# Kernel tuning notes

Measured on AMD Instinct MI355X. Metric: run time of the kernel, lower is better.

Reference implementation:

```python
import jax, jax.numpy as jnp
import numpy as np

N_NODES = 100000
N_EDGES = 600000
EMB = 128
L = 5
NUM_ATOM = 119
NUM_CHIR = 3
NUM_BTYPE = 5
NUM_BDIR = 3
BN_EPS = 1e-5


def setup_inputs() -> dict:
    key = jax.random.key(0)
    ks = jax.random.split(key, 16)
    inp = {}
    inp['x'] = jax.random.randint(ks[0], (N_NODES, 2), 0, NUM_ATOM, dtype=jnp.int64 if jax.config.jax_enable_x64 else jnp.int32)
    inp['edge_index'] = jax.random.randint(ks[1], (2, N_EDGES), 0, N_NODES)
    inp['edge_attr'] = jax.random.randint(ks[2], (N_EDGES, 2), 0, NUM_BDIR)
    s = 0.05
    inp['x_emb1'] = jax.random.normal(ks[3], (NUM_ATOM, EMB), jnp.float32) * s
    inp['x_emb2'] = jax.random.normal(ks[4], (NUM_CHIR, EMB), jnp.float32) * s
    inp['edge_emb1'] = jax.random.normal(ks[5], (L, NUM_BTYPE, EMB), jnp.float32) * s
    inp['edge_emb2'] = jax.random.normal(ks[6], (L, NUM_BDIR, EMB), jnp.float32) * s
    inp['W1'] = jax.random.normal(ks[7], (L, EMB, 2 * EMB), jnp.float32) * (1.0 / np.sqrt(EMB))
    inp['b1'] = jnp.zeros((L, 2 * EMB), jnp.float32)
    inp['W2'] = jax.random.normal(ks[8], (L, 2 * EMB, EMB), jnp.float32) * (1.0 / np.sqrt(2 * EMB))
    inp['b2'] = jnp.zeros((L, EMB), jnp.float32)
    inp['eps'] = jnp.zeros((L,), jnp.float32)
    inp['gamma'] = jnp.ones((L, EMB), jnp.float32)
    inp['beta'] = jnp.zeros((L, EMB), jnp.float32)
    return inp


def reference(x, edge_index, edge_attr, x_emb1, x_emb2, edge_emb1, edge_emb2,
              W1, b1, W2, b2, eps, gamma, beta):
    N = x.shape[0]
    # node embedding: sum of two table lookups
    x0 = jnp.clip(x[:, 0], 0, x_emb1.shape[0] - 1)
    x1 = jnp.clip(x[:, 1], 0, x_emb2.shape[0] - 1)
    h = x_emb1[x0] + x_emb2[x1]  # [N, EMB]
    # add self loops (loop edge_attr = zeros -> bond type 0 / dir 0)
    loop = jnp.arange(N, dtype=edge_index.dtype)
    src = jnp.concatenate([edge_index[0], loop])  # [E+N]
    dst = jnp.concatenate([edge_index[1], loop])
    ea = jnp.concatenate([edge_attr, jnp.zeros((N, 2), dtype=edge_attr.dtype)], axis=0)
    e0 = jnp.clip(ea[:, 0], 0, edge_emb1.shape[1] - 1)
    e1 = jnp.clip(ea[:, 1], 0, edge_emb2.shape[1] - 1)
    n_layers = eps.shape[0]
    for i in range(n_layers):
        e = edge_emb1[i][e0] + edge_emb2[i][e1]              # [E+N, EMB]
        m = jax.nn.relu(h[src] + e)                           # gather + elementwise
        agg = jax.ops.segment_sum(m, dst, num_segments=N)     # scatter-add
        out = (1.0 + eps[i]) * h + agg
        # MLP: Linear -> ReLU -> Linear
        hmid = jax.nn.relu(out @ W1[i] + b1[i])
        h = hmid @ W2[i] + b2[i]
        # BatchNorm1d over nodes (batch statistics, biased variance)
        mean = jnp.mean(h, axis=0)
        var = jnp.mean((h - mean) ** 2, axis=0)
        h = (h - mean) * jax.lax.rsqrt(var + BN_EPS) * gamma[i] + beta[i]
        if i < n_layers - 1:
            h = jax.nn.relu(h)
    return h
```

## Files before the change

### kernel.cpp

```cpp
#include <hip/hip_runtime.h>

#define NN 100000
#define NPAD 100096
#define NE 600000
#define EMB 128

typedef unsigned short u16;
typedef unsigned int u32;
typedef unsigned long long u64;
typedef _Float16 half8 __attribute__((ext_vector_type(8)));
typedef float f32x4 __attribute__((ext_vector_type(4)));

__device__ __forceinline__ float4 ld4(const float* p) { return *(const float4*)p; }
__device__ __forceinline__ u32 packh2(float a, float b) {
  union { _Float16 h[2]; u32 d; } u;
  u.h[0] = (_Float16)a;
  u.h[1] = (_Float16)b;
  return u.d;
}

__global__ __launch_bounds__(256) void node_init_kernel(
    const int* __restrict__ x, const float* __restrict__ emb1,
    const float* __restrict__ emb2, _Float16* __restrict__ hb) {
  int tid = blockIdx.x * blockDim.x + threadIdx.x;
  int n = tid >> 4;
  if (n >= NN) return;
  int kc = tid & 15;
  int x0 = min(max(x[2 * n], 0), 118);
  int x1 = min(max(x[2 * n + 1], 0), 2);
  const float* p1 = emb1 + (size_t)x0 * EMB + kc * 8;
  const float* p2 = emb2 + (size_t)x1 * EMB + kc * 8;
  _Float16 o[8];
#pragma unroll
  for (int j = 0; j < 8; ++j) o[j] = (_Float16)(p1[j] + p2[j]);
  *(ulonglong2*)(hb + (size_t)n * EMB + kc * 8) = *(ulonglong2*)o;
}

__global__ __launch_bounds__(256) void hist_kernel(const int* __restrict__ ei,
                                                   int* __restrict__ deg) {
  int e = blockIdx.x * blockDim.x + threadIdx.x;
  if (e >= NE) return;
  atomicAdd(&deg[ei[NE + e]], 1);
}

__global__ __launch_bounds__(256) void scan1_kernel(const int* __restrict__ deg,
                                                    int* __restrict__ off,
                                                    int* __restrict__ bsum,
                                                    int* __restrict__ gbins) {
  __shared__ int s[256];
  __shared__ int l[33];
  int t = threadIdx.x;
  if (t < 33) l[t] = 0;
  int base = blockIdx.x * 1024 + t * 4;
  int v[4];
#pragma unroll
  for (int j = 0; j < 4; ++j) {
    int idx = base + j;
    v[j] = (idx < NN) ? deg[idx] : 0;
  }
  int tsum = v[0] + v[1] + v[2] + v[3];
  s[t] = tsum;
  __syncthreads();
  for (int d = 1; d < 256; d <<= 1) {
    int add = (t >= d) ? s[t - d] : 0;
    __syncthreads();
    s[t] += add;
    __syncthreads();
  }
  int run = s[t] - tsum;
#pragma unroll
  for (int j = 0; j < 4; ++j) {
    int idx = base + j;
    if (idx < NN) {
      off[idx] = run;
      atomicAdd(&l[32 - min(v[j], 32)], 1);
    }
    run += v[j];
  }
  if (t == 255) bsum[blockIdx.x] = s[255];
  __syncthreads();
  if (t < 33 && l[t]) atomicAdd(&gbins[t], l[t]);
}

__global__ void scan2_kernel(int* __restrict__ bsum, int* __restrict__ off, int nb,
                             int* __restrict__ gbins) {
  int t = threadIdx.x;
  if (t < 64) {
    int lane = t;
    int v0 = (lane < nb) ? bsum[lane] : 0;
    int v1 = (lane + 64 < nb) ? bsum[lane + 64] : 0;
    int s0 = v0, s1 = v1;
    for (int d = 1; d < 64; d <<= 1) {
      int t0 = __shfl_up(s0, d);
      int t1 = __shfl_up(s1, d);
      if (lane >= d) { s0 += t0; s1 += t1; }
    }
    int tot0 = __shfl(s0, 63);
    int tot1 = __shfl(s1, 63);
    if (lane < nb) bsum[lane] = s0 - v0;
    if (lane + 64 < nb) bsum[lane + 64] = tot0 + s1 - v1;
    if (lane == 0) off[NN] = tot0 + tot1;
  } else {
    int lane = t - 64;
    int v = (lane < 33) ? gbins[lane] : 0;
    int s = v;
    for (int d = 1; d < 64; d <<= 1) {
      int tt = __shfl_up(s, d);
      if (lane >= d) s += tt;
    }
    if (lane < 33) gbins[lane] = s - v;
  }
}

__global__ __launch_bounds__(256) void scan3_kernel(int* __restrict__ off,
                                                    const int* __restrict__ bsum,
                                                    const int* __restrict__ deg,
                                                    int* __restrict__ gbins,
                                                    int* __restrict__ perm) {
  __shared__ int lcnt[33], lbase[33];
  int t = threadIdx.x;
  if (t < 33) lcnt[t] = 0;
  __syncthreads();
  int idx = blockIdx.x * 256 + t;
  int b = 0, r = 0;
  if (idx < NN) {
    off[idx] += bsum[idx >> 10];
    b = 32 - min(deg[idx], 32);
    r = atomicAdd(&lcnt[b], 1);
  }
  __syncthreads();
  if (t < 33) lbase[t] = lcnt[t] ? atomicAdd(&gbins[t], lcnt[t]) : 0;
  __syncthreads();
  if (idx < NN) perm[lbase[b] + r] = idx;
}

__global__ __launch_bounds__(256) void scatter_kernel(
    const int* __restrict__ ei, const int* __restrict__ ea,
    const int* __restrict__ off, int* __restrict__ cnt, int* __restrict__ csr) {
  int e = blockIdx.x * blockDim.x + threadIdx.x;
  if (e >= NE) return;
  int d = ei[NE + e];
  int s = ei[e];
  int a0 = min(max(ea[2 * e], 0), 4);
  int a1 = min(max(ea[2 * e + 1], 0), 2);
  int code = a0 * 3 + a1;
  int r = atomicAdd(&cnt[d], 1);
  csr[off[d] + r] = s | (code << 20);
}

__global__ __launch_bounds__(256) void prep_kernel(
    const float* __restrict__ W1g, const float* __restrict__ W2g,
    const float* __restrict__ ee1, const float* __restrict__ ee2,
    _Float16* __restrict__ W1f, _Float16* __restrict__ W2f,
    _Float16* __restrict__ cbh) {
  int idx = blockIdx.x * blockDim.x + threadIdx.x;
  _Float16 o[8];
  if (idx < 20480) {
    int lane = idx & 63;
    int r = idx >> 6;
    int nt = r & 3, kt = (r >> 2) & 3, c = (r >> 4) & 3, l = r >> 6;
    int n = c * 64 + nt * 16 + (lane & 15);
    int kb = kt * 32 + (lane >> 4) * 8;
#pragma unroll
    for (int j = 0; j < 8; ++j) o[j] = (_Float16)W1g[((size_t)l * 128 + kb + j) * 256 + n];
    *(ulonglong2*)(W1f + (size_t)idx * 8) = *(ulonglong2*)o;
  } else if (idx < 40960) {
    int i2 = idx - 20480;
    int lane = i2 & 63;
    int r = i2 >> 6;
    int nt = r & 7, ktl = (r >> 3) & 1, c = (r >> 4) & 3, l = r >> 6;
    int n = nt * 16 + (lane & 15);
    int kb = c * 64 + ktl * 32 + (lane >> 4) * 8;
#pragma unroll
    for (int j = 0; j < 8; ++j) o[j] = (_Float16)W2g[((size_t)l * 256 + kb + j) * 128 + n];
    *(ulonglong2*)(W2f + (size_t)i2 * 8) = *(ulonglong2*)o;
  } else if (idx < 40960 + 9600) {
    int i3 = idx - 40960;
    int l = i3 / (15 * 128);
    int rem = i3 % (15 * 128);
    int code = rem / 128;
    int f = rem % 128;
    cbh[i3] = (_Float16)(ee1[(l * 5 + code / 3) * 128 + f] + ee2[(l * 3 + code % 3) * 128 + f]);
  }
}

template <bool NORM>
__global__ __launch_bounds__(256) void agg_kernel(
    const _Float16* __restrict__ hsrc, const float* __restrict__ slots,
    const float* __restrict__ gamma, const float* __restrict__ beta,
    const int* __restrict__ off, const int* __restrict__ csr,
    const _Float16* __restrict__ cbh, const float* __restrict__ epsp,
    const int* __restrict__ perm, _Float16* __restrict__ Af) {
  __shared__ float s_sc[128], s_sh[128];
  int t = threadIdx.x;
  if (NORM) {
    if (t < 128) {
      float s = 0.f, s2 = 0.f;
#pragma unroll 8
      for (int k = 0; k < 32; ++k) {
        s += slots[k * 256 + t];
        s2 += slots[k * 256 + 128 + t];
      }
      float mean = s * (1.0f / NN);
      float var = s2 * (1.0f / NN) - mean * mean;
      float sc = gamma[t] * rsqrtf(var + 1e-5f);
      s_sc[t] = sc;
      s_sh[t] = beta[t] - mean * sc;
    }
    __syncthreads();
  }
  int tid = blockIdx.x * blockDim.x + t;
  int g = tid >> 4;
  int kc = tid & 15;
  float av[8] = {0.f, 0.f, 0.f, 0.f, 0.f, 0.f, 0.f, 0.f};
  float scv[8], shv[8];
  if (NORM) {
#pragma unroll
    for (int j = 0; j < 8; ++j) {
      scv[j] = s_sc[kc * 8 + j];
      shv[j] = s_sh[kc * 8 + j];
    }
  }
  int node = g;
  if (g < NN) {
    node = perm[g];
    const float eps1 = 1.0f + *epsp;
    ulonglong2 hraw = *(const ulonglong2*)(hsrc + (size_t)node * EMB + kc * 8);
    _Float16* hr = (_Float16*)&hraw;
    half8 c0 = *(const half8*)(cbh + kc * 8);
#pragma unroll
    for (int j = 0; j < 8; ++j) {
      float hv = (float)hr[j];
      if (NORM) hv = fmaxf(hv * scv[j] + shv[j], 0.f);
      av[j] = eps1 * hv + fmaxf(hv + (float)c0[j], 0.f);
    }
    int s0 = off[node], s1 = off[node + 1];
    int e = s0;
    for (; e + 3 < s1; e += 4) {
      int p0 = csr[e], p1 = csr[e + 1], p2 = csr[e + 2], p3 = csr[e + 3];
      ulonglong2 r0 = *(const ulonglong2*)(hsrc + (size_t)(p0 & 0xFFFFF) * EMB + kc * 8);
      ulonglong2 r1 = *(const ulonglong2*)(hsrc + (size_t)(p1 & 0xFFFFF) * EMB + kc * 8);
      ulonglong2 r2 = *(const ulonglong2*)(hsrc + (size_t)(p2 & 0xFFFFF) * EMB + kc * 8);
      ulonglong2 r3 = *(const ulonglong2*)(hsrc + (size_t)(p3 & 0xFFFFF) * EMB + kc * 8);
      ulonglong2 rr[4] = {r0, r1, r2, r3};
      int pp[4] = {p0, p1, p2, p3};
#pragma unroll
      for (int u = 0; u < 4; ++u) {
        half8 cc = *(const half8*)(cbh + (size_t)(pp[u] >> 20) * EMB + kc * 8);
        _Float16* sp = (_Float16*)&rr[u];
#pragma unroll
        for (int j = 0; j < 8; ++j) {
          float v = (float)sp[j];
          if (NORM) v = fmaxf(v * scv[j] + shv[j], 0.f);
          av[j] += fmaxf(v + (float)cc[j], 0.f);
        }
      }
    }
    for (; e < s1; ++e) {
      int p0 = csr[e];
      ulonglong2 r0 = *(const ulonglong2*)(hsrc + (size_t)(p0 & 0xFFFFF) * EMB + kc * 8);
      half8 cc = *(const half8*)(cbh + (size_t)(p0 >> 20) * EMB + kc * 8);
      _Float16* sp = (_Float16*)&r0;
#pragma unroll
      for (int j = 0; j < 8; ++j) {
        float v = (float)sp[j];
        if (NORM) v = fmaxf(v * scv[j] + shv[j], 0.f);
        av[j] += fmaxf(v + (float)cc[j], 0.f);
      }
    }
  }
  _Float16 o[8];
#pragma unroll
  for (int j = 0; j < 8; ++j) o[j] = (_Float16)av[j];
  *(ulonglong2*)(Af + (size_t)node * EMB + kc * 8) = *(ulonglong2*)o;
}

__global__ __launch_bounds__(256, 4) void mlp_kernel(
    const _Float16* __restrict__ Af, const _Float16* __restrict__ W1f,
    const _Float16* __restrict__ W2f,
    const float* __restrict__ b1g, const float* __restrict__ b2g,
    _Float16* __restrict__ hpre, float* __restrict__ slots) {
  __shared__ __align__(16) _Float16 Ws[16 * 64 * 8];

  const int t = threadIdx.x;
  const int w = t >> 6;
  const int lane = t & 63;
  const int q = lane >> 4, l15 = lane & 15;
  const int gw = blockIdx.x * 4 + w;
  const int n0 = gw * 16;
  float* sums = slots + (size_t)(gw & 31) * 256;

  half8 nh[4];
#pragma unroll
  for (int kt = 0; kt < 4; ++kt)
    nh[kt] = *(const half8*)(Af + (size_t)(n0 + l15) * EMB + kt * 32 + q * 8);

  f32x4 oacc[8];
#pragma unroll
  for (int a = 0; a < 8; ++a) oacc[a] = (f32x4){0.f, 0.f, 0.f, 0.f};

  const int srcA = ((q & 1) * 2) * 16 + l15;
  const int srcB = srcA + 16;
  const bool sel = (q >> 1) != 0;

  for (int c = 0; c < 4; ++c) {
    __syncthreads();
    {
      const _Float16* gb = W1f + ((size_t)(c * 16 + w * 4) * 64 + lane) * 8;
#pragma unroll
      for (int j = 0; j < 4; ++j)
        *(ulonglong2*)&Ws[(w * 4 + j) * 512 + lane * 8] =
            *(const ulonglong2*)(gb + (size_t)j * 512);
    }
    __syncthreads();

    f32x4 hacc[4];
#pragma unroll
    for (int a = 0; a < 4; ++a) hacc[a] = (f32x4){0.f, 0.f, 0.f, 0.f};
#pragma unroll
    for (int kt = 0; kt < 4; ++kt) {
#pragma unroll
      for (int colt = 0; colt < 4; ++colt) {
        half8 wh = *(const half8*)&Ws[(kt * 4 + colt) * 512 + lane * 8];
        hacc[colt] = __builtin_amdgcn_mfma_f32_16x16x32_f16(wh, nh[kt], hacc[colt], 0, 0, 0);
      }
    }
    __syncthreads();

    {
      const _Float16* gb = W2f + ((size_t)(c * 16 + w * 4) * 64 + lane) * 8;
#pragma unroll
      for (int j = 0; j < 4; ++j)
        *(ulonglong2*)&Ws[(w * 4 + j) * 512 + lane * 8] =
            *(const ulonglong2*)(gb + (size_t)j * 512);
    }

    u32 P01[4], P23[4];
#pragma unroll
    for (int colt = 0; colt < 4; ++colt) {
      float4 b1v = ld4(b1g + c * 64 + colt * 16 + q * 4);
      float v0 = fmaxf(hacc[colt][0] + b1v.x, 0.f);
      float v1 = fmaxf(hacc[colt][1] + b1v.y, 0.f);
      float v2 = fmaxf(hacc[colt][2] + b1v.z, 0.f);
      float v3 = fmaxf(hacc[colt][3] + b1v.w, 0.f);
      P01[colt] = packh2(v0, v1);
      P23[colt] = packh2(v2, v3);
    }
    __syncthreads();

#pragma unroll
    for (int ktl = 0; ktl < 2; ++ktl) {
      half8 bh;
      {
        union { u32 d[4]; half8 s; } uh;
        int c0 = 2 * ktl, c1 = 2 * ktl + 1;
        u32 a0, a1;
        a0 = (u32)__shfl((int)P01[c0], srcA); a1 = (u32)__shfl((int)P01[c1], srcA);
        uh.d[0] = sel ? a1 : a0;
        a0 = (u32)__shfl((int)P23[c0], srcA); a1 = (u32)__shfl((int)P23[c1], srcA);
        uh.d[1] = sel ? a1 : a0;
        a0 = (u32)__shfl((int)P01[c0], srcB); a1 = (u32)__shfl((int)P01[c1], srcB);
        uh.d[2] = sel ? a1 : a0;
        a0 = (u32)__shfl((int)P23[c0], srcB); a1 = (u32)__shfl((int)P23[c1], srcB);
        uh.d[3] = sel ? a1 : a0;
        bh = uh.s;
      }
#pragma unroll
      for (int nt = 0; nt < 8; ++nt) {
        half8 wh = *(const half8*)&Ws[(ktl * 8 + nt) * 512 + lane * 8];
        oacc[nt] = __builtin_amdgcn_mfma_f32_16x16x32_f16(wh, bh, oacc[nt], 0, 0, 0);
      }
    }
  }

  const int node = n0 + l15;
#pragma unroll
  for (int nt = 0; nt < 8; ++nt) {
    int ocb = nt * 16 + q * 4;
    float4 b2v = ld4(b2g + ocb);
    f32x4 s = (f32x4){0.f, 0.f, 0.f, 0.f};
    f32x4 s2 = (f32x4){0.f, 0.f, 0.f, 0.f};
    if (node < NN) {
      float v0 = oacc[nt][0] + b2v.x;
      float v1 = oacc[nt][1] + b2v.y;
      float v2 = oacc[nt][2] + b2v.z;
      float v3 = oacc[nt][3] + b2v.w;
      u64 pk = (u64)packh2(v0, v1) | ((u64)packh2(v2, v3) << 32);
      *(u64*)(hpre + (size_t)node * EMB + ocb) = pk;
      s[0] = v0; s[1] = v1; s[2] = v2; s[3] = v3;
      s2[0] = v0 * v0; s2[1] = v1 * v1; s2[2] = v2 * v2; s2[3] = v3 * v3;
    }
#pragma unroll
    for (int d = 1; d < 16; d <<= 1) {
#pragma unroll
      for (int r = 0; r < 4; ++r) {
        s[r] += __shfl_xor(s[r], d);
        s2[r] += __shfl_xor(s2[r], d);
      }
    }
    if (l15 == 0) {
#pragma unroll
      for (int r = 0; r < 4; ++r) {
        atomicAdd(&sums[ocb + r], s[r]);
        atomicAdd(&sums[128 + ocb + r], s2[r]);
      }
    }
  }
}

__global__ __launch_bounds__(256) void out_kernel(
    const _Float16* __restrict__ hpre, const float* __restrict__ slots,
    const float* __restrict__ gamma, const float* __restrict__ beta,
    float* __restrict__ out) {
  __shared__ float s_sc[128], s_sh[128];
  int t = threadIdx.x;
  if (t < 128) {
    float s = 0.f, s2 = 0.f;
#pragma unroll 8
    for (int k = 0; k < 32; ++k) {
      s += slots[k * 256 + t];
      s2 += slots[k * 256 + 128 + t];
    }
    float mean = s * (1.0f / NN);
    float var = s2 * (1.0f / NN) - mean * mean;
    float sc = gamma[t] * rsqrtf(var + 1e-5f);
    s_sc[t] = sc;
    s_sh[t] = beta[t] - mean * sc;
  }
  __syncthreads();
  int tid = blockIdx.x * blockDim.x + t;
  int n = tid >> 4;
  if (n >= NN) return;
  int kc = tid & 15;
  ulonglong2 raw = *(const ulonglong2*)(hpre + (size_t)n * EMB + kc * 8);
  _Float16* hr = (_Float16*)&raw;
  float v[8];
#pragma unroll
  for (int j = 0; j < 8; ++j) v[j] = (float)hr[j] * s_sc[kc * 8 + j] + s_sh[kc * 8 + j];
  float* d = out + (size_t)n * EMB + kc * 8;
  *(float4*)d = make_float4(v[0], v[1], v[2], v[3]);
  *(float4*)(d + 4) = make_float4(v[4], v[5], v[6], v[7]);
}

extern "C" void kernel_launch(void* const* d_in, const int* in_sizes, int n_in,
                              void* d_out, int out_size, void* d_ws, size_t ws_size,
                              hipStream_t stream) {
  const int* x = (const int*)d_in[0];
  const int* ei = (const int*)d_in[1];
  const int* ea = (const int*)d_in[2];
  const float* x_emb1 = (const float*)d_in[3];
  const float* x_emb2 = (const float*)d_in[4];
  const float* ee1 = (const float*)d_in[5];
  const float* ee2 = (const float*)d_in[6];
  const float* W1 = (const float*)d_in[7];
  const float* b1 = (const float*)d_in[8];
  const float* W2 = (const float*)d_in[9];
  const float* b2 = (const float*)d_in[10];
  const float* eps = (const float*)d_in[11];
  const float* gamma = (const float*)d_in[12];
  const float* beta = (const float*)d_in[13];
  float* out = (float*)d_out;

  float* slots = (float*)d_ws;
  _Float16* hpre = (_Float16*)(slots + 5 * 32 * 256);
  _Float16* Af = hpre + (size_t)NN * EMB;
  _Float16* hb = Af + (size_t)NPAD * EMB;
  _Float16* W1f = hb + (size_t)NN * EMB;
  _Float16* W2f = W1f + 5 * 32768;
  _Float16* cbh = W2f + 5 * 32768;
  int* deg = (int*)(cbh + 5 * 15 * 128 + 64);
  int* off = deg + NN;
  int* csr = off + NN + 1;
  int* bsum = csr + NE;
  int* gbins = bsum + 128;
  int* perm = gbins + 64;

  const int NB_SCAN = (NN + 1023) / 1024;

  hipMemsetAsync(deg, 0, NN * sizeof(int), stream);
  hipMemsetAsync(gbins, 0, 64 * sizeof(int), stream);
  hipMemsetAsync(slots, 0, 5 * 32 * 256 * sizeof(float), stream);
  hist_kernel<<<(NE + 255) / 256, 256, 0, stream>>>(ei, deg);
  scan1_kernel<<<NB_SCAN, 256, 0, stream>>>(deg, off, bsum, gbins);
  scan2_kernel<<<1, 128, 0, stream>>>(bsum, off, NB_SCAN, gbins);
  scan3_kernel<<<(NN + 255) / 256, 256, 0, stream>>>(off, bsum, deg, gbins, perm);
  hipMemsetAsync(deg, 0, NN * sizeof(int), stream);
  scatter_kernel<<<(NE + 255) / 256, 256, 0, stream>>>(ei, ea, off, deg, csr);
  prep_kernel<<<(40960 + 9600 + 255) / 256, 256, 0, stream>>>(W1, W2, ee1, ee2, W1f,
                                                              W2f, cbh);
  node_init_kernel<<<NN * 16 / 256 + 1, 256, 0, stream>>>(x, x_emb1, x_emb2, hb);

  const int NBLK = NPAD / 64;
  for (int i = 0; i < 5; ++i) {
    if (i == 0)
      agg_kernel<false><<<NPAD * 16 / 256, 256, 0, stream>>>(
          hb, nullptr, nullptr, nullptr, off, csr, cbh + (size_t)i * 15 * EMB,
          eps + i, perm, Af);
    else
      agg_kernel<true><<<NPAD * 16 / 256, 256, 0, stream>>>(
          hpre, slots + (size_t)(i - 1) * 32 * 256, gamma + (size_t)(i - 1) * EMB,
          beta + (size_t)(i - 1) * EMB, off, csr, cbh + (size_t)i * 15 * EMB,
          eps + i, perm, Af);
    mlp_kernel<<<NBLK, 256, 0, stream>>>(
        Af, W1f + (size_t)i * 32768, W2f + (size_t)i * 32768,
        b1 + (size_t)i * 256, b2 + (size_t)i * 128, hpre,
        slots + (size_t)i * 32 * 256);
  }
  out_kernel<<<NN * 16 / 256 + 1, 256, 0, stream>>>(
      hpre, slots + 4 * 32 * 256, gamma + 4 * EMB, beta + 4 * EMB, out);
}
```

Baseline: 651.2 us.

## Fuse neighbor aggregation into MLP kernel via shared-memory staging

Merges the gather/aggregate kernel into the MLP kernel. Each wave aggregates its 16 nodes straight into LDS, and the MFMA operands are loaded from LDS instead of a global Af buffer. Ping-pong hidden-state buffers avoid read/write hazards now that aggregation and output share one kernel. This removes the Af round-trip to global memory and one launch per layer. The cost is less parallelism and latency hiding for the irregular gather inside a register-heavy MFMA kernel.

```diff
diff --git a/kernel.cpp b/kernel.cpp
--- a/kernel.cpp
+++ b/kernel.cpp
@@ -185,102 +185,17 @@
 }
 
 template <bool NORM>
-__global__ __launch_bounds__(256) void agg_kernel(
-    const _Float16* __restrict__ hsrc, const float* __restrict__ slots,
+__global__ __launch_bounds__(256, 4) void fused_kernel(
+    const _Float16* __restrict__ hsrc, const float* __restrict__ slots_prev,
     const float* __restrict__ gamma, const float* __restrict__ beta,
     const int* __restrict__ off, const int* __restrict__ csr,
     const _Float16* __restrict__ cbh, const float* __restrict__ epsp,
-    const int* __restrict__ perm, _Float16* __restrict__ Af) {
+    const int* __restrict__ perm,
+    const _Float16* __restrict__ W1f, const _Float16* __restrict__ W2f,
+    const float* __restrict__ b1g, const float* __restrict__ b2g,
+    _Float16* __restrict__ hout, float* __restrict__ slots_out) {
+  __shared__ __align__(16) _Float16 Ws[16 * 64 * 8];
   __shared__ float s_sc[128], s_sh[128];
-  int t = threadIdx.x;
-  if (NORM) {
-    if (t < 128) {
-      float s = 0.f, s2 = 0.f;
-#pragma unroll 8
-      for (int k = 0; k < 32; ++k) {
-        s += slots[k * 256 + t];
-        s2 += slots[k * 256 + 128 + t];
-      }
-      float mean = s * (1.0f / NN);
-      float var = s2 * (1.0f / NN) - mean * mean;
-      float sc = gamma[t] * rsqrtf(var + 1e-5f);
-      s_sc[t] = sc;
-      s_sh[t] = beta[t] - mean * sc;
-    }
-    __syncthreads();
-  }
-  int tid = blockIdx.x * blockDim.x + t;
-  int g = tid >> 4;
-  int kc = tid & 15;
-  float av[8] = {0.f, 0.f, 0.f, 0.f, 0.f, 0.f, 0.f, 0.f};
-  float scv[8], shv[8];
-  if (NORM) {
-#pragma unroll
-    for (int j = 0; j < 8; ++j) {
-      scv[j] = s_sc[kc * 8 + j];
-      shv[j] = s_sh[kc * 8 + j];
-    }
-  }
-  int node = g;
-  if (g < NN) {
-    node = perm[g];
-    const float eps1 = 1.0f + *epsp;
-    ulonglong2 hraw = *(const ulonglong2*)(hsrc + (size_t)node * EMB + kc * 8);
-    _Float16* hr = (_Float16*)&hraw;
-    half8 c0 = *(const half8*)(cbh + kc * 8);
-#pragma unroll
-    for (int j = 0; j < 8; ++j) {
-      float hv = (float)hr[j];
-      if (NORM) hv = fmaxf(hv * scv[j] + shv[j], 0.f);
-      av[j] = eps1 * hv + fmaxf(hv + (float)c0[j], 0.f);
-    }
-    int s0 = off[node], s1 = off[node + 1];
-    int e = s0;
-    for (; e + 3 < s1; e += 4) {
-      int p0 = csr[e], p1 = csr[e + 1], p2 = csr[e + 2], p3 = csr[e + 3];
-      ulonglong2 r0 = *(const ulonglong2*)(hsrc + (size_t)(p0 & 0xFFFFF) * EMB + kc * 8);
-      ulonglong2 r1 = *(const ulonglong2*)(hsrc + (size_t)(p1 & 0xFFFFF) * EMB + kc * 8);
-      ulonglong2 r2 = *(const ulonglong2*)(hsrc + (size_t)(p2 & 0xFFFFF) * EMB + kc * 8);
-      ulonglong2 r3 = *(const ulonglong2*)(hsrc + (size_t)(p3 & 0xFFFFF) * EMB + kc * 8);
-      ulonglong2 rr[4] = {r0, r1, r2, r3};
-      int pp[4] = {p0, p1, p2, p3};
-#pragma unroll
-      for (int u = 0; u < 4; ++u) {
-        half8 cc = *(const half8*)(cbh + (size_t)(pp[u] >> 20) * EMB + kc * 8);
-        _Float16* sp = (_Float16*)&rr[u];
-#pragma unroll
-        for (int j = 0; j < 8; ++j) {
-          float v = (float)sp[j];
-          if (NORM) v = fmaxf(v * scv[j] + shv[j], 0.f);
-          av[j] += fmaxf(v + (float)cc[j], 0.f);
-        }
-      }
-    }
-    for (; e < s1; ++e) {
-      int p0 = csr[e];
-      ulonglong2 r0 = *(const ulonglong2*)(hsrc + (size_t)(p0 & 0xFFFFF) * EMB + kc * 8);
-      half8 cc = *(const half8*)(cbh + (size_t)(p0 >> 20) * EMB + kc * 8);
-      _Float16* sp = (_Float16*)&r0;
-#pragma unroll
-      for (int j = 0; j < 8; ++j) {
-        float v = (float)sp[j];
-        if (NORM) v = fmaxf(v * scv[j] + shv[j], 0.f);
-        av[j] += fmaxf(v + (float)cc[j], 0.f);
-      }
-    }
-  }
-  _Float16 o[8];
-#pragma unroll
-  for (int j = 0; j < 8; ++j) o[j] = (_Float16)av[j];
-  *(ulonglong2*)(Af + (size_t)node * EMB + kc * 8) = *(ulonglong2*)o;
-}
-
-__global__ __launch_bounds__(256, 4) void mlp_kernel(
-    const _Float16* __restrict__ Af, const _Float16* __restrict__ W1f,
-    const _Float16* __restrict__ W2f,
-    const float* __restrict__ b1g, const float* __restrict__ b2g,
-    _Float16* __restrict__ hpre, float* __restrict__ slots) {
-  __shared__ __align__(16) _Float16 Ws[16 * 64 * 8];
 
   const int t = threadIdx.x;
   const int w = t >> 6;
@@ -288,12 +203,97 @@
   const int q = lane >> 4, l15 = lane & 15;
   const int gw = blockIdx.x * 4 + w;
   const int n0 = gw * 16;
-  float* sums = slots + (size_t)(gw & 31) * 256;
+  float* sums = slots_out + (size_t)(gw & 31) * 256;
+
+  if (NORM) {
+    if (t < 128) {
+      float s = 0.f, s2 = 0.f;
+#pragma unroll 8
+      for (int k = 0; k < 32; ++k) {
+        s += slots_prev[k * 256 + t];
+        s2 += slots_prev[k * 256 + 128 + t];
+      }
+      float mean = s * (1.0f / NN);
+      float var = s2 * (1.0f / NN) - mean * mean;
+      float sc = gamma[t] * rsqrtf(var + 1e-5f);
+      s_sc[t] = sc;
+      s_sh[t] = beta[t] - mean * sc;
+    }
+    __syncthreads();
+  }
+
+  {
+    const int sub = q;
+    const int kc = l15;
+    float scv[8], shv[8];
+    if (NORM) {
+#pragma unroll
+      for (int j = 0; j < 8; ++j) {
+        scv[j] = s_sc[kc * 8 + j];
+        shv[j] = s_sh[kc * 8 + j];
+      }
+    }
+    const float eps1 = 1.0f + *epsp;
+    half8 c0 = *(const half8*)(cbh + kc * 8);
+    for (int p = 0; p < 4; ++p) {
+      int g = n0 + p * 4 + sub;
+      float av[8] = {0.f, 0.f, 0.f, 0.f, 0.f, 0.f, 0.f, 0.f};
+      if (g < NN) {
+        int node = perm[g];
+        ulonglong2 hraw = *(const ulonglong2*)(hsrc + (size_t)node * EMB + kc * 8);
+        _Float16* hr = (_Float16*)&hraw;
+#pragma unroll
+        for (int j = 0; j < 8; ++j) {
+          float hv = (float)hr[j];
+          if (NORM) hv = fmaxf(hv * scv[j] + shv[j], 0.f);
+          av[j] = eps1 * hv + fmaxf(hv + (float)c0[j], 0.f);
+        }
+        int s0 = off[node], s1 = off[node + 1];
+        int e = s0;
+        for (; e + 3 < s1; e += 4) {
+          int p0 = csr[e], p1 = csr[e + 1], p2 = csr[e + 2], p3 = csr[e + 3];
+          ulonglong2 r0 = *(const ulonglong2*)(hsrc + (size_t)(p0 & 0xFFFFF) * EMB + kc * 8);
+          ulonglong2 r1 = *(const ulonglong2*)(hsrc + (size_t)(p1 & 0xFFFFF) * EMB + kc * 8);
+          ulonglong2 r2 = *(const ulonglong2*)(hsrc + (size_t)(p2 & 0xFFFFF) * EMB + kc * 8);
+          ulonglong2 r3 = *(const ulonglong2*)(hsrc + (size_t)(p3 & 0xFFFFF) * EMB + kc * 8);
+          ulonglong2 rr[4] = {r0, r1, r2, r3};
+          int pp[4] = {p0, p1, p2, p3};
+#pragma unroll
+          for (int u = 0; u < 4; ++u) {
+            half8 cc = *(const half8*)(cbh + (size_t)(pp[u] >> 20) * EMB + kc * 8);
+            _Float16* sp = (_Float16*)&rr[u];
+#pragma unroll
+            for (int j = 0; j < 8; ++j) {
+              float v = (float)sp[j];
+              if (NORM) v = fmaxf(v * scv[j] + shv[j], 0.f);
+              av[j] += fmaxf(v + (float)cc[j], 0.f);
+            }
+          }
+        }
+        for (; e < s1; ++e) {
+          int p0 = csr[e];
+          ulonglong2 r0 = *(const ulonglong2*)(hsrc + (size_t)(p0 & 0xFFFFF) * EMB + kc * 8);
+          half8 cc = *(const half8*)(cbh + (size_t)(p0 >> 20) * EMB + kc * 8);
+          _Float16* sp = (_Float16*)&r0;
+#pragma unroll
+          for (int j = 0; j < 8; ++j) {
+            float v = (float)sp[j];
+            if (NORM) v = fmaxf(v * scv[j] + shv[j], 0.f);
+            av[j] += fmaxf(v + (float)cc[j], 0.f);
+          }
+        }
+      }
+      _Float16 o[8];
+#pragma unroll
+      for (int j = 0; j < 8; ++j) o[j] = (_Float16)av[j];
+      *(ulonglong2*)&Ws[w * 2048 + (p * 4 + sub) * 128 + kc * 8] = *(ulonglong2*)o;
+    }
+  }
 
   half8 nh[4];
 #pragma unroll
   for (int kt = 0; kt < 4; ++kt)
-    nh[kt] = *(const half8*)(Af + (size_t)(n0 + l15) * EMB + kt * 32 + q * 8);
+    nh[kt] = *(const half8*)&Ws[w * 2048 + l15 * 128 + kt * 32 + q * 8];
 
   f32x4 oacc[8];
 #pragma unroll
@@ -373,20 +373,22 @@
     }
   }
 
-  const int node = n0 + l15;
+  const int gg = n0 + l15;
+  const bool ok = gg < NN;
+  const int node = ok ? perm[gg] : 0;
 #pragma unroll
   for (int nt = 0; nt < 8; ++nt) {
     int ocb = nt * 16 + q * 4;
     float4 b2v = ld4(b2g + ocb);
     f32x4 s = (f32x4){0.f, 0.f, 0.f, 0.f};
     f32x4 s2 = (f32x4){0.f, 0.f, 0.f, 0.f};
-    if (node < NN) {
+    if (ok) {
       float v0 = oacc[nt][0] + b2v.x;
       float v1 = oacc[nt][1] + b2v.y;
       float v2 = oacc[nt][2] + b2v.z;
       float v3 = oacc[nt][3] + b2v.w;
       u64 pk = (u64)packh2(v0, v1) | ((u64)packh2(v2, v3) << 32);
-      *(u64*)(hpre + (size_t)node * EMB + ocb) = pk;
+      *(u64*)(hout + (size_t)node * EMB + ocb) = pk;
       s[0] = v0; s[1] = v1; s[2] = v2; s[3] = v3;
       s2[0] = v0 * v0; s2[1] = v1 * v1; s2[2] = v2 * v2; s2[3] = v3 * v3;
     }
@@ -462,9 +464,9 @@
   float* out = (float*)d_out;
 
   float* slots = (float*)d_ws;
-  _Float16* hpre = (_Float16*)(slots + 5 * 32 * 256);
-  _Float16* Af = hpre + (size_t)NN * EMB;
-  _Float16* hb = Af + (size_t)NPAD * EMB;
+  _Float16* hp0 = (_Float16*)(slots + 5 * 32 * 256);
+  _Float16* hp1 = hp0 + (size_t)NN * EMB;
+  _Float16* hb = hp1 + (size_t)NN * EMB;
   _Float16* W1f = hb + (size_t)NN * EMB;
   _Float16* W2f = W1f + 5 * 32768;
   _Float16* cbh = W2f + 5 * 32768;
@@ -492,20 +494,20 @@
 
   const int NBLK = NPAD / 64;
   for (int i = 0; i < 5; ++i) {
+    const _Float16* hin = (i == 0) ? hb : ((i & 1) ? hp0 : hp1);
+    _Float16* hout = (i & 1) ? hp1 : hp0;
     if (i == 0)
-      agg_kernel<false><<<NPAD * 16 / 256, 256, 0, stream>>>(
-          hb, nullptr, nullptr, nullptr, off, csr, cbh + (size_t)i * 15 * EMB,
-          eps + i, perm, Af);
+      fused_kernel<false><<<NBLK, 256, 0, stream>>>(
+          hin, nullptr, nullptr, nullptr, off, csr, cbh, eps, perm,
+          W1f, W2f, b1, b2, hout, slots);
     else
-      agg_kernel<true><<<NPAD * 16 / 256, 256, 0, stream>>>(
-          hpre, slots + (size_t)(i - 1) * 32 * 256, gamma + (size_t)(i - 1) * EMB,
+      fused_kernel<true><<<NBLK, 256, 0, stream>>>(
+          hin, slots + (size_t)(i - 1) * 32 * 256, gamma + (size_t)(i - 1) * EMB,
           beta + (size_t)(i - 1) * EMB, off, csr, cbh + (size_t)i * 15 * EMB,
-          eps + i, perm, Af);
-    mlp_kernel<<<NBLK, 256, 0, stream>>>(
-        Af, W1f + (size_t)i * 32768, W2f + (size_t)i * 32768,
-        b1 + (size_t)i * 256, b2 + (size_t)i * 128, hpre,
-        slots + (size_t)i * 32 * 256);
+          eps + i, perm, W1f + (size_t)i * 32768, W2f + (size_t)i * 32768,
+          b1 + (size_t)i * 256, b2 + (size_t)i * 128, hout,
+          slots + (size_t)i * 32 * 256);
   }
   out_kernel<<<NN * 16 / 256 + 1, 256, 0, stream>>>(
-      hpre, slots + 4 * 32 * 256, gamma + 4 * EMB, beta + 4 * EMB, out);
-}
+      hp0, slots + 4 * 32 * 256, gamma + 4 * EMB, beta + 4 * EMB, out);
+}
```

After: 601.4 us. -7.6%, faster.
